# Optimization experiments

Hardware: AMD Instinct MI355X
Metric: run time of the kernel (lower is better)

## Reference

```python
import jax, jax.numpy as jnp
import numpy as np

B, T, C, H = 4, 4096, 1024, 64


def setup_inputs() -> dict:
    key = jax.random.key(0)
    kx, kk, kq, kv = jax.random.split(key, 4)
    x = jax.random.normal(kx, (B, T, C), dtype=jnp.float32)
    # bias-free linear weights, stored as [in, out] so y = x @ W
    Wk = jax.random.normal(kk, (C, H), dtype=jnp.float32) * (C ** -0.5)
    Wq = jax.random.normal(kq, (C, H), dtype=jnp.float32) * (C ** -0.5)
    Wv = jax.random.normal(kv, (C, H), dtype=jnp.float32) * (C ** -0.5)
    return {"x": x, "Wk": Wk, "Wq": Wq, "Wv": Wv}


def reference(x, Wk, Wq, Wv):
    b, t, c = x.shape
    k = x @ Wk  # [B,T,H]
    q = x @ Wq
    v = x @ Wv
    # NOTE: original scales by C**-0.5 (num_embed), not head_size**-0.5
    wei = jnp.einsum('bqh,bkh->bqk', q, k) * (c ** -0.5)  # [B,T,T]
    causal = jnp.tril(jnp.ones((t, t), dtype=bool))
    wei = jnp.where(causal, wei, -jnp.inf)
    wei = jax.nn.softmax(wei, axis=-1)
    # dropout p=0.0 (eval) -> identity
    return jnp.einsum('bqk,bkh->bqh', wei, v)  # [B,T,H]
```

## Files before the change

### kernel.cpp

```cpp
#include <hip/hip_runtime.h>
#include <hip/hip_bf16.h>

typedef unsigned short u16;
typedef unsigned int u32;
using f32x4 = __attribute__((ext_vector_type(4))) float;
using s16x8 = __attribute__((ext_vector_type(8))) short;

#define BATCH 4
#define SEQ   4096
#define CDIM  1024
#define HDIM  64
#define QT_N  256

__device__ inline u16 f32_to_bf16(float f) {
    u32 u = __builtin_bit_cast(u32, f);
    u += 0x7FFFu + ((u >> 16) & 1u);
    return (u16)(u >> 16);
}
__device__ inline u32 pkbf16(float a, float b) {
    return (u32)f32_to_bf16(a) | ((u32)f32_to_bf16(b) << 16);
}
__device__ inline f32x4 mfma16(s16x8 a, s16x8 b, f32x4 c) {
    return __builtin_amdgcn_mfma_f32_16x16x32_bf16(a, b, c, 0, 0, 0);
}


__global__ __launch_bounds__(64) void wtrans_kernel(
        const float* __restrict__ Wk, const float* __restrict__ Wq,
        const float* __restrict__ Wv, u16* __restrict__ Wtf) {
    int bx = blockIdx.x;
    int nt = bx >> 5, kc = bx & 31;
    int lane = threadIdx.x;
    int l16 = lane & 15, qd = lane >> 4;
    int n = nt * 16 + l16;
    int a = n >> 6, h = n & 63;
    const float* src = (a == 0) ? Wk : (a == 1) ? Wq : Wv;
    float scale = (a == 1) ? 0.045084220027780106f : 1.0f;
    u32 p[4];
#pragma unroll
    for (int pp = 0; pp < 4; ++pp) {
        int k = kc * 32 + qd * 8 + pp * 2;
        p[pp] = pkbf16(src[k * HDIM + h] * scale, src[(k + 1) * HDIM + h] * scale);
    }
    uint4 u; u.x = p[0]; u.y = p[1]; u.z = p[2]; u.w = p[3];
    *(uint4*)&Wtf[(size_t)((nt * 32 + kc) * 64 + lane) * 8] = u;
}

__global__ __launch_bounds__(256, 4) void proj_kernel(
        const float* __restrict__ x, const u16* __restrict__ Wtf,
        u16* __restrict__ qf, u16* __restrict__ kf, u16* __restrict__ vf) {
    __shared__ __align__(16) u16 xs[16][1032];
    int t = threadIdx.x, lane = t & 63, w = t >> 6;
    int quad = lane >> 4, l16 = lane & 15;
    int row0 = blockIdx.x * 16;

    const float* xb = x + (size_t)row0 * CDIM;
#pragma unroll 4
    for (int i = 0; i < 16; ++i) {
        float4 f = *(const float4*)(xb + (size_t)i * CDIM + t * 4);
        uint2 u; u.x = pkbf16(f.x, f.y); u.y = pkbf16(f.z, f.w);
        *(uint2*)&xs[i][t * 4] = u;
    }
    __syncthreads();

    f32x4 acc[3];
#pragma unroll
    for (int n = 0; n < 3; ++n) acc[n] = (f32x4){0.f, 0.f, 0.f, 0.f};

#pragma unroll 4
    for (int kc = 0; kc < 32; ++kc) {
        s16x8 a0 = *(const s16x8*)&xs[l16][kc * 32 + quad * 8];
#pragma unroll
        for (int n = 0; n < 3; ++n) {
            int nt = w * 3 + n;
            s16x8 b = *(const s16x8*)&Wtf[(size_t)((nt * 32 + kc) * 64 + lane) * 8];
            acc[n] = mfma16(a0, b, acc[n]);
        }
    }
    int rbase = row0 + quad * 4;
    int bb = rbase >> 12, rl = rbase & 4095;
#pragma unroll
    for (int n = 0; n < 3; ++n) {
        int n0 = w * 48 + n * 16;
        if (n0 < 128) {
            u16* dst = (n0 < 64) ? kf : qf;
            int h = (n0 & 63) + l16;
            int tt16 = rl >> 4, hc = h >> 5, qd2 = (h >> 3) & 3, j = h & 7;
            size_t base = ((size_t)((bb * 256 + tt16) * 2 + hc) * 64
                           + qd2 * 16 + (rl & 15)) * 8 + j;
#pragma unroll
            for (int r = 0; r < 4; ++r)
                dst[base + (size_t)r * 8] = f32_to_bf16(acc[n][r]);
        } else {
            int h0 = n0 - 128;
            int ht = h0 >> 4;
            int kc2 = rl >> 5, qdv = (rl >> 3) & 3, j0 = rl & 7;
            u32 lo = pkbf16(acc[n][0], acc[n][1]);
            u32 hi = pkbf16(acc[n][2], acc[n][3]);
            size_t base = ((size_t)((bb * 128 + kc2) * 4 + ht) * 64
                           + qdv * 16 + l16) * 8 + j0;
            uint2 u; u.x = lo; u.y = hi;
            *(uint2*)&vf[base] = u;
        }
    }
}

__global__ __launch_bounds__(512, 4) void flash_kernel(
        const u16* __restrict__ qf, const u16* __restrict__ kf,
        const u16* __restrict__ vf, float* __restrict__ out) {
    __shared__ float cb[8][32][68];
    __shared__ float lb[8][32];
    int t = threadIdx.x, w = t >> 6, lane = t & 63;
    int quad = lane >> 4, l16 = lane & 15;
    int bx = blockIdx.x;
    int b = bx & 3;
    int j = (bx & 255) >> 2;
    int qt2 = (bx < 256) ? (127 - j) : j;

    const u16* qp0 = qf + ((size_t)((b * QT_N + qt2 * 2) * 2) * 64 + lane) * 8;
    const u16* qp1 = qp0 + 2 * 64 * 8;
    s16x8 bq[2][2];
    bq[0][0] = *(const s16x8*)qp0;
    bq[0][1] = *(const s16x8*)(qp0 + 512);
    bq[1][0] = *(const s16x8*)qp1;
    bq[1][1] = *(const s16x8*)(qp1 + 512);
    s16x8 ones;
#pragma unroll
    for (int jj = 0; jj < 8; ++jj) ones[jj] = (short)0x3F80;

    f32x4 o[2][4], o5[2];
#pragma unroll
    for (int tl = 0; tl < 2; ++tl) {
        o5[tl] = (f32x4){0.f, 0.f, 0.f, 0.f};
#pragma unroll
        for (int i = 0; i < 4; ++i) o[tl][i] = (f32x4){0.f, 0.f, 0.f, 0.f};
    }

    int nb = (qt2 * 32 + 32 + 63) >> 6;
    int iters = (nb + 7) >> 3;
    int rowq0 = qt2 * 32 + l16;
    const u16* kfb = kf + (size_t)b * 256 * 2 * 512;
    const u16* vfb = vf + (size_t)b * 128 * 4 * 512;
    int a0 = ((quad & 1) * 32 + l16) * 4;
    int a1 = a0 + 64;
    u32 msk = (quad < 2) ? 0xFFFFFFFFu : 0u;

    auto iteration = [&](int kb, bool domask) {
        f32x4 sT[2][4];
#pragma unroll
        for (int kt = 0; kt < 4; ++kt) {
            const u16* kp = kfb + ((size_t)((kb * 4 + kt) * 2) * 64 + lane) * 8;
            s16x8 k0 = *(const s16x8*)kp;
            s16x8 k1 = *(const s16x8*)(kp + 512);
            f32x4 z = (f32x4){0.f, 0.f, 0.f, 0.f};
            sT[0][kt] = mfma16(k1, bq[0][1], mfma16(k0, bq[0][0], z));
            sT[1][kt] = mfma16(k1, bq[1][1], mfma16(k0, bq[1][0], z));
        }
        u32 P01[2][4], P23[2][4];
#pragma unroll
        for (int tl = 0; tl < 2; ++tl) {
            int rowq = rowq0 + tl * 16;
#pragma unroll
            for (int kt = 0; kt < 4; ++kt) {
                float e[4];
#pragma unroll
                for (int r = 0; r < 4; ++r) {
                    float ev = __builtin_amdgcn_exp2f(sT[tl][kt][r]);
                    if (domask) {
                        int key = kb * 64 + kt * 16 + quad * 4 + r;
                        ev = (key > rowq) ? 0.f : ev;
                    }
                    e[r] = ev;
                }
                P01[tl][kt] = pkbf16(e[0], e[1]);
                P23[tl][kt] = pkbf16(e[2], e[3]);
            }
        }
#pragma unroll
        for (int c = 0; c < 2; ++c) {
            s16x8 vA[4];
#pragma unroll
            for (int ht = 0; ht < 4; ++ht)
                vA[ht] = *(const s16x8*)&vfb[((size_t)((kb * 2 + c) * 4 + ht) * 64
                                             + lane) * 8];
            int t0 = 2 * c, t1 = 2 * c + 1;
#pragma unroll
            for (int tl = 0; tl < 2; ++tl) {
                u32 x0 = (u32)__builtin_amdgcn_ds_bpermute(a0, (int)P01[tl][t0]);
                u32 y0 = (u32)__builtin_amdgcn_ds_bpermute(a0, (int)P01[tl][t1]);
                u32 x1 = (u32)__builtin_amdgcn_ds_bpermute(a0, (int)P23[tl][t0]);
                u32 y1 = (u32)__builtin_amdgcn_ds_bpermute(a0, (int)P23[tl][t1]);
                u32 x2 = (u32)__builtin_amdgcn_ds_bpermute(a1, (int)P01[tl][t0]);
                u32 y2 = (u32)__builtin_amdgcn_ds_bpermute(a1, (int)P01[tl][t1]);
                u32 x3 = (u32)__builtin_amdgcn_ds_bpermute(a1, (int)P23[tl][t0]);
                u32 y3 = (u32)__builtin_amdgcn_ds_bpermute(a1, (int)P23[tl][t1]);
                uint4 pu;
                pu.x = (x0 & msk) | (y0 & ~msk);
                pu.y = (x1 & msk) | (y1 & ~msk);
                pu.z = (x2 & msk) | (y2 & ~msk);
                pu.w = (x3 & msk) | (y3 & ~msk);
                s16x8 pb = __builtin_bit_cast(s16x8, pu);
#pragma unroll
                for (int ht = 0; ht < 4; ++ht)
                    o[tl][ht] = mfma16(vA[ht], pb, o[tl][ht]);
                o5[tl] = mfma16(ones, pb, o5[tl]);
            }
        }
    };

    for (int i = 0; i < iters - 1; ++i) iteration(8 * i + w, false);
    {
        int kb = 8 * (iters - 1) + w;
        if (kb < nb) iteration(kb, true);
    }
#pragma unroll
    for (int tl = 0; tl < 2; ++tl) {
#pragma unroll
        for (int ht = 0; ht < 4; ++ht)
#pragma unroll
            for (int r = 0; r < 4; ++r)
                cb[w][tl * 16 + l16][ht * 16 + quad * 4 + r] = o[tl][ht][r];
        if (quad == 0) lb[w][tl * 16 + l16] = o5[tl][0];
    }
    __syncthreads();
    int row = t >> 4, c0 = (t & 15) * 4;
    float l = 0.f;
    float4 s = (float4){0.f, 0.f, 0.f, 0.f};
#pragma unroll
    for (int w8 = 0; w8 < 8; ++w8) {
        l += lb[w8][row];
        float4 p = *(const float4*)&cb[w8][row][c0];
        s.x += p.x; s.y += p.y; s.z += p.z; s.w += p.w;
    }
    float rcp = 1.0f / l;
    s.x *= rcp; s.y *= rcp; s.z *= rcp; s.w *= rcp;
    *(float4*)&out[((size_t)(b * SEQ) + qt2 * 32 + row) * HDIM + c0] = s;
}

extern "C" void kernel_launch(void* const* d_in, const int* in_sizes, int n_in,
                              void* d_out, int out_size, void* d_ws, size_t ws_size,
                              hipStream_t stream) {
    const float* x  = (const float*)d_in[0];
    const float* Wk = (const float*)d_in[1];
    const float* Wq = (const float*)d_in[2];
    const float* Wv = (const float*)d_in[3];
    u16* wsu = (u16*)d_ws;
    u16* Wtf = wsu;
    u16* kf  = Wtf + 196608;
    u16* qf  = kf + 1048576;
    u16* vf  = qf + 1048576;
    float* out = (float*)d_out;

    hipLaunchKernelGGL(wtrans_kernel, dim3(384), dim3(64), 0, stream, Wk, Wq, Wv, Wtf);
    hipLaunchKernelGGL(proj_kernel, dim3(1024), dim3(256), 0, stream, x, Wtf, qf, kf, vf);
    hipLaunchKernelGGL(flash_kernel, dim3((SEQ / 32) * BATCH), dim3(512), 0, stream,
                       qf, kf, vf, out);
}
```

Baseline: 128.6 us.

## Double proj_kernel row tile to 32 rows with 512 threads sharing weight fragments

The projection kernel now handles 32 rows per block with 8 waves instead of 16 rows with 4 waves. Each wave computes a 2x2-interleaved set of three 16x16 output tiles, so every weight fragment loaded from global memory feeds two MFMAs. The x staging loads use wider 8-float chunks. This aims to cut weight-fragment reloads and halve the block count, at the cost of doubled LDS per block (about 66 KB), which may lower occupancy.

```diff
diff --git a/kernel.cpp b/kernel.cpp
--- a/kernel.cpp
+++ b/kernel.cpp
@@ -46,20 +46,24 @@
     *(uint4*)&Wtf[(size_t)((nt * 32 + kc) * 64 + lane) * 8] = u;
 }
 
-__global__ __launch_bounds__(256, 4) void proj_kernel(
+__global__ __launch_bounds__(512, 4) void proj_kernel(
         const float* __restrict__ x, const u16* __restrict__ Wtf,
         u16* __restrict__ qf, u16* __restrict__ kf, u16* __restrict__ vf) {
-    __shared__ __align__(16) u16 xs[16][1032];
+    __shared__ __align__(16) u16 xs[32][1032];
     int t = threadIdx.x, lane = t & 63, w = t >> 6;
     int quad = lane >> 4, l16 = lane & 15;
-    int row0 = blockIdx.x * 16;
+    int row0 = blockIdx.x * 32;
 
     const float* xb = x + (size_t)row0 * CDIM;
 #pragma unroll 4
-    for (int i = 0; i < 16; ++i) {
-        float4 f = *(const float4*)(xb + (size_t)i * CDIM + t * 4);
-        uint2 u; u.x = pkbf16(f.x, f.y); u.y = pkbf16(f.z, f.w);
-        *(uint2*)&xs[i][t * 4] = u;
+    for (int i = 0; i < 8; ++i) {
+        int flat = i * 4096 + t * 8;
+        float4 f0 = *(const float4*)(xb + flat);
+        float4 f1 = *(const float4*)(xb + flat + 4);
+        uint4 u;
+        u.x = pkbf16(f0.x, f0.y); u.y = pkbf16(f0.z, f0.w);
+        u.z = pkbf16(f1.x, f1.y); u.w = pkbf16(f1.z, f1.w);
+        *(uint4*)&xs[flat >> 10][flat & 1023] = u;
     }
     __syncthreads();
 
@@ -67,21 +71,41 @@
 #pragma unroll
     for (int n = 0; n < 3; ++n) acc[n] = (f32x4){0.f, 0.f, 0.f, 0.f};
 
+    int nt_lo = (3 * w) >> 1;
+    const u16* bp0 = Wtf + ((size_t)(nt_lo * 32) * 64 + lane) * 8;
+    const u16* bp1 = bp0 + (size_t)32 * 64 * 8;
+
+    if ((w & 1) == 0) {
 #pragma unroll 4
-    for (int kc = 0; kc < 32; ++kc) {
-        s16x8 a0 = *(const s16x8*)&xs[l16][kc * 32 + quad * 8];
-#pragma unroll
-        for (int n = 0; n < 3; ++n) {
-            int nt = w * 3 + n;
-            s16x8 b = *(const s16x8*)&Wtf[(size_t)((nt * 32 + kc) * 64 + lane) * 8];
-            acc[n] = mfma16(a0, b, acc[n]);
-        }
-    }
-    int rbase = row0 + quad * 4;
-    int bb = rbase >> 12, rl = rbase & 4095;
-#pragma unroll
-    for (int n = 0; n < 3; ++n) {
-        int n0 = w * 48 + n * 16;
+        for (int kc = 0; kc < 32; ++kc) {
+            s16x8 a0 = *(const s16x8*)&xs[l16][kc * 32 + quad * 8];
+            s16x8 a1 = *(const s16x8*)&xs[16 + l16][kc * 32 + quad * 8];
+            s16x8 b0 = *(const s16x8*)(bp0 + (size_t)kc * 512);
+            s16x8 b1 = *(const s16x8*)(bp1 + (size_t)kc * 512);
+            acc[0] = mfma16(a0, b0, acc[0]);
+            acc[1] = mfma16(a1, b0, acc[1]);
+            acc[2] = mfma16(a0, b1, acc[2]);
+        }
+    } else {
+#pragma unroll 4
+        for (int kc = 0; kc < 32; ++kc) {
+            s16x8 a0 = *(const s16x8*)&xs[l16][kc * 32 + quad * 8];
+            s16x8 a1 = *(const s16x8*)&xs[16 + l16][kc * 32 + quad * 8];
+            s16x8 b0 = *(const s16x8*)(bp0 + (size_t)kc * 512);
+            s16x8 b1 = *(const s16x8*)(bp1 + (size_t)kc * 512);
+            acc[0] = mfma16(a1, b0, acc[0]);
+            acc[1] = mfma16(a0, b1, acc[1]);
+            acc[2] = mfma16(a1, b1, acc[2]);
+        }
+    }
+
+#pragma unroll
+    for (int i = 0; i < 3; ++i) {
+        int u = 3 * w + i;
+        int nt = u >> 1, rh = u & 1;
+        int n0 = nt * 16;
+        int rbase = row0 + rh * 16 + quad * 4;
+        int bb = rbase >> 12, rl = rbase & 4095;
         if (n0 < 128) {
             u16* dst = (n0 < 64) ? kf : qf;
             int h = (n0 & 63) + l16;
@@ -90,17 +114,16 @@
                            + qd2 * 16 + (rl & 15)) * 8 + j;
 #pragma unroll
             for (int r = 0; r < 4; ++r)
-                dst[base + (size_t)r * 8] = f32_to_bf16(acc[n][r]);
+                dst[base + (size_t)r * 8] = f32_to_bf16(acc[i][r]);
         } else {
-            int h0 = n0 - 128;
-            int ht = h0 >> 4;
+            int ht = (n0 - 128) >> 4;
             int kc2 = rl >> 5, qdv = (rl >> 3) & 3, j0 = rl & 7;
-            u32 lo = pkbf16(acc[n][0], acc[n][1]);
-            u32 hi = pkbf16(acc[n][2], acc[n][3]);
+            u32 lo = pkbf16(acc[i][0], acc[i][1]);
+            u32 hi = pkbf16(acc[i][2], acc[i][3]);
             size_t base = ((size_t)((bb * 128 + kc2) * 4 + ht) * 64
                            + qdv * 16 + l16) * 8 + j0;
-            uint2 u; u.x = lo; u.y = hi;
-            *(uint2*)&vf[base] = u;
+            uint2 u2; u2.x = lo; u2.y = hi;
+            *(uint2*)&vf[base] = u2;
         }
     }
 }
@@ -252,7 +275,7 @@
     float* out = (float*)d_out;
 
     hipLaunchKernelGGL(wtrans_kernel, dim3(384), dim3(64), 0, stream, Wk, Wq, Wv, Wtf);
-    hipLaunchKernelGGL(proj_kernel, dim3(1024), dim3(256), 0, stream, x, Wtf, qf, kf, vf);
+    hipLaunchKernelGGL(proj_kernel, dim3(512), dim3(512), 0, stream, x, Wtf, qf, kf, vf);
     hipLaunchKernelGGL(flash_kernel, dim3((SEQ / 32) * BATCH), dim3(512), 0, stream,
                        qf, kf, vf, out);
 }
```

Result: no change. 126.8 us (-1.4%).
